# Optimization experiments

Measured on AMD Instinct MI355X. Metric: run time of the kernel, lower is better.

Reference implementation:

```python
import jax, jax.numpy as jnp
import numpy as np

B, T, D, H = 2, 2048, 1024, 16
DH = D // H

def setup_inputs() -> dict:
    key = jax.random.key(0)
    ks = jax.random.split(key, 5)
    s = 1.0 / np.sqrt(D)
    return {
        "x": jax.random.normal(ks[0], (B, T, D), dtype=jnp.float32),
        "w_q": jax.random.normal(ks[1], (D, D), dtype=jnp.float32) * s,
        "w_k": jax.random.normal(ks[2], (D, D), dtype=jnp.float32) * s,
        "w_v": jax.random.normal(ks[3], (D, D), dtype=jnp.float32) * s,
        "w_o": jax.random.normal(ks[4], (D, D), dtype=jnp.float32) * s,
    }

def reference(x, w_q, w_k, w_v, w_o):
    # Linear(bias=False): y = x @ W.T
    q = jnp.einsum('btd,ed->bte', x, w_q).reshape(B, T, H, DH).transpose(0, 2, 1, 3)
    k = jnp.einsum('btd,ed->bte', x, w_k).reshape(B, T, H, DH).transpose(0, 2, 1, 3)
    v = jnp.einsum('btd,ed->bte', x, w_v).reshape(B, T, H, DH).transpose(0, 2, 1, 3)
    scores = jnp.einsum('bhqd,bhkd->bhqk', q, k) / np.sqrt(DH)  # [B,H,T,T]
    causal = jnp.triu(jnp.ones((T, T), dtype=bool), k=1)
    scores = jnp.where(causal[None, None, :, :], -jnp.inf, scores)
    attn = jax.nn.softmax(scores, axis=-1)
    ctx = jnp.einsum('bhqk,bhkd->bhqd', attn, v)
    ctx = ctx.transpose(0, 2, 1, 3).reshape(B, T, D)
    out = jnp.einsum('btd,ed->bte', ctx, w_o)
    return out
```

## Files before the change

### kernel.cpp

```cpp
#include <hip/hip_runtime.h>
#include <hip/hip_bf16.h>

typedef __bf16 bf16_t;
typedef __attribute__((ext_vector_type(8))) __bf16 bf16x8;
typedef __attribute__((ext_vector_type(4))) __bf16 bf16x4;
typedef __attribute__((ext_vector_type(4))) float f32x4;
typedef __attribute__((ext_vector_type(16))) float f32x16;
typedef __attribute__((ext_vector_type(2))) int i32x2;

#define B_ 2
#define T_ 2048
#define D_ 1024
#define H_ 16
#define DH_ 64
#define RS_ 3072

static __device__ __forceinline__ f32x4 mfma16(bf16x8 a, bf16x8 b, f32x4 c) {
  return __builtin_amdgcn_mfma_f32_16x16x32_bf16(a, b, c, 0, 0, 0);
}
static __device__ __forceinline__ f32x16 mfma32(bf16x8 a, bf16x8 b, f32x16 c) {
  return __builtin_amdgcn_mfma_f32_32x32x16_bf16(a, b, c, 0, 0, 0);
}
static __device__ __forceinline__ void gld16(const bf16_t* g, bf16_t* l) {
  __builtin_amdgcn_global_load_lds(
      (const __attribute__((address_space(1))) unsigned int*)g,
      (__attribute__((address_space(3))) unsigned int*)l, 16, 0, 0);
}
static __device__ __forceinline__ unsigned lds_addr(const bf16_t* p) {
  return (unsigned)(uintptr_t)(const __attribute__((address_space(3))) bf16_t*)p;
}
static __device__ __forceinline__ i32x2 tr64(unsigned a) {
  i32x2 d;
  asm volatile("ds_read_b64_tr_b16 %0, %1" : "=v"(d) : "v"(a));
  return d;
}
static __device__ __forceinline__ i32x2 tr64o(unsigned a) {
  i32x2 d;
  asm volatile("ds_read_b64_tr_b16 %0, %1 offset:128" : "=v"(d) : "v"(a));
  return d;
}
static __device__ __forceinline__ unsigned pk2(float lo, float hi2) {
  unsigned short a = __builtin_bit_cast(unsigned short, (bf16_t)lo);
  unsigned short b = __builtin_bit_cast(unsigned short, (bf16_t)hi2);
  return (unsigned)a | ((unsigned)b << 16);
}

#define WAITV3 { asm volatile("s_waitcnt vmcnt(3)" ::: "memory"); __builtin_amdgcn_sched_barrier(0); }
#define WAITV4 { asm volatile("s_waitcnt vmcnt(4)" ::: "memory"); __builtin_amdgcn_sched_barrier(0); }
#define WAITV0 { asm volatile("s_waitcnt vmcnt(0)" ::: "memory"); __builtin_amdgcn_sched_barrier(0); }
#define BAR    { __builtin_amdgcn_s_barrier(); __builtin_amdgcn_sched_barrier(0); }
#define WAITL0 { asm volatile("s_waitcnt lgkmcnt(0)" ::: "memory"); __builtin_amdgcn_sched_barrier(0); }

__global__ __launch_bounds__(256) void cvt_all(const float* __restrict__ x,
                                               const float* __restrict__ w0,
                                               const float* __restrict__ w1,
                                               const float* __restrict__ w2,
                                               const float* __restrict__ w3,
                                               bf16_t* __restrict__ out) {
  const int y = blockIdx.y;
  const float* in = (y < 4) ? (x + (size_t)y * 1048576)
                            : (y == 4 ? w0 : y == 5 ? w1 : y == 6 ? w2 : w3);
  bf16_t* o = out + (size_t)y * 1048576;
  int i = blockIdx.x * 256 + threadIdx.x;
  float4 f = reinterpret_cast<const float4*>(in)[i];
  bf16x4 v;
  v[0] = (bf16_t)f.x; v[1] = (bf16_t)f.y; v[2] = (bf16_t)f.z; v[3] = (bf16_t)f.w;
  reinterpret_cast<bf16x4*>(o)[i] = v;
}

template <bool STORE_F32, bool QSCALE>
__global__ __launch_bounds__(256) void gemm_nt(const bf16_t* __restrict__ A,
                                               const bf16_t* __restrict__ Bm,
                                               void* __restrict__ Cv,
                                               int M, int N, int K, int nbx) {
  __shared__ __align__(16) bf16_t As[3][128 * 32];
  __shared__ __align__(16) bf16_t Bs[3][128 * 32];
  const int id = blockIdx.x;
  const int nwg = gridDim.x;
  const int cpx = nwg >> 3;
  const int swz = (id & 7) * cpx + (id >> 3);
  const int bx = swz % nbx, by = swz / nbx;
  const int tid = threadIdx.x, lane = tid & 63, wave = tid >> 6;
  const int l15 = lane & 15;
  const int brow = by * 128, bcol = bx * 128;
  const int row0 = (wave >> 1) * 64, col0 = (wave & 1) * 64;
  const float cscale = (QSCALE && bcol < 1024) ? 0.18033688011112042f : 1.0f;

  f32x4 acc[4][4];
#pragma unroll
  for (int m = 0; m < 4; ++m)
#pragma unroll
    for (int n = 0; n < 4; ++n) acc[m][n] = f32x4{0.f, 0.f, 0.f, 0.f};

  const int nst = K >> 5;
  const int srow = tid >> 2;
  const int sc8 = (tid & 3) * 8;
  auto stage = [&](int bi, int ks) {
    const int k0 = ks * 32;
#pragma unroll
    for (int i = 0; i < 2; ++i)
      gld16(A + (size_t)(brow + 64 * i + srow) * K + k0 + sc8,
            &As[bi][2048 * i + 512 * wave]);
#pragma unroll
    for (int i = 0; i < 2; ++i)
      gld16(Bm + (size_t)(bcol + 64 * i + srow) * K + k0 + sc8,
            &Bs[bi][2048 * i + 512 * wave]);
  };

  stage(0, 0);
  stage(1, 1);

#pragma unroll 1
  for (int ks = 0; ks < nst; ++ks) {
    if (ks + 1 < nst) { WAITV4 } else { WAITV0 }
    BAR;
    if (ks + 2 < nst) stage((ks + 2) % 3, ks + 2);

    const bf16_t* Ab = &As[ks % 3][0];
    const bf16_t* Bb = &Bs[ks % 3][0];
    const int ko = (lane >> 4) * 8;
    bf16x8 af[4], bfr[4];
#pragma unroll
    for (int m = 0; m < 4; ++m)
      af[m] = *(const bf16x8*)&Ab[(row0 + 16 * m + l15) * 32 + ko];
#pragma unroll
    for (int n = 0; n < 4; ++n)
      bfr[n] = *(const bf16x8*)&Bb[(col0 + 16 * n + l15) * 32 + ko];
    WAITL0;
#pragma unroll
    for (int m = 0; m < 4; ++m)
#pragma unroll
      for (int n = 0; n < 4; ++n) acc[m][n] = mfma16(af[m], bfr[n], acc[m][n]);
  }

  const int crow = brow + row0 + (lane >> 4) * 4;
  const int ccol = bcol + col0 + l15;
#pragma unroll
  for (int m = 0; m < 4; ++m)
#pragma unroll
    for (int n = 0; n < 4; ++n)
#pragma unroll
      for (int r = 0; r < 4; ++r) {
        size_t idx = (size_t)(crow + 16 * m + r) * N + (ccol + 16 * n);
        float v = acc[m][n][r] * cscale;
        if (STORE_F32) reinterpret_cast<float*>(Cv)[idx] = v;
        else reinterpret_cast<bf16_t*>(Cv)[idx] = (bf16_t)v;
      }
}

__global__ __launch_bounds__(256) void gemm_nt64(const bf16_t* __restrict__ A,
                                                 const bf16_t* __restrict__ Bm,
                                                 float* __restrict__ Cv,
                                                 int M, int N, int K, int nbx) {
  __shared__ __align__(16) bf16_t As[3][64 * 32];
  __shared__ __align__(16) bf16_t Bs[3][128 * 32];
  const int id = blockIdx.x;
  const int cpx = gridDim.x >> 3;
  const int swz = (id & 7) * cpx + (id >> 3);
  const int bx = swz % nbx, by = swz / nbx;
  const int tid = threadIdx.x, lane = tid & 63, wave = tid >> 6;
  const int l15 = lane & 15;
  const int brow = by * 64, bcol = bx * 128;
  const int row0 = (wave >> 1) * 32, col0 = (wave & 1) * 64;

  f32x4 acc[2][4];
#pragma unroll
  for (int m = 0; m < 2; ++m)
#pragma unroll
    for (int n = 0; n < 4; ++n) acc[m][n] = f32x4{0.f, 0.f, 0.f, 0.f};

  const int nst = K >> 5;
  const int sr = lane >> 2;
  const int sc8 = (lane & 3) * 8;
  auto stage = [&](int bi, int ks) {
    const int k0 = ks * 32;
    gld16(A + (size_t)(brow + 16 * wave + sr) * K + k0 + sc8, &As[bi][512 * wave]);
#pragma unroll
    for (int i = 0; i < 2; ++i)
      gld16(Bm + (size_t)(bcol + 64 * i + 16 * wave + sr) * K + k0 + sc8,
            &Bs[bi][2048 * i + 512 * wave]);
  };

  stage(0, 0);
  stage(1, 1);

#pragma unroll 1
  for (int ks = 0; ks < nst; ++ks) {
    if (ks + 1 < nst) { WAITV3 } else { WAITV0 }
    BAR;
    if (ks + 2 < nst) stage((ks + 2) % 3, ks + 2);

    const bf16_t* Ab = &As[ks % 3][0];
    const bf16_t* Bb = &Bs[ks % 3][0];
    const int ko = (lane >> 4) * 8;
    bf16x8 af[2], bfr[4];
#pragma unroll
    for (int m = 0; m < 2; ++m)
      af[m] = *(const bf16x8*)&Ab[(row0 + 16 * m + l15) * 32 + ko];
#pragma unroll
    for (int n = 0; n < 4; ++n)
      bfr[n] = *(const bf16x8*)&Bb[(col0 + 16 * n + l15) * 32 + ko];
    WAITL0;
#pragma unroll
    for (int m = 0; m < 2; ++m)
#pragma unroll
      for (int n = 0; n < 4; ++n) acc[m][n] = mfma16(af[m], bfr[n], acc[m][n]);
  }

  const int crow = brow + row0 + (lane >> 4) * 4;
  const int ccol = bcol + col0 + l15;
#pragma unroll
  for (int m = 0; m < 2; ++m)
#pragma unroll
    for (int n = 0; n < 4; ++n)
#pragma unroll
      for (int r = 0; r < 4; ++r)
        Cv[(size_t)(crow + 16 * m + r) * N + (ccol + 16 * n)] = acc[m][n][r];
}

#define CROW(r) ((((r) & 3) + 8 * ((r) >> 2)) + 4 * hi)

__global__ __launch_bounds__(256, 1) void attn_fwd(const bf16_t* __restrict__ qkv,
                                                   bf16_t* __restrict__ ctx) {
  __shared__ __align__(128) bf16_t KV[3][2][64 * 64];
  const int tid = threadIdx.x;
  const int lane = tid & 63;
  const int wv = tid >> 6;
  const int bh = blockIdx.x, p = blockIdx.y;
  const int b = bh >> 4, h = bh & 15;
  const bf16_t* Qg = qkv + (size_t)b * T_ * RS_ + h * DH_;
  const bf16_t* Kg = Qg + 1024;
  const bf16_t* Vg = Qg + 2048;
  bf16_t* Cg = ctx + (size_t)b * T_ * D_ + h * DH_;

  const int hi = lane >> 5;
  const int l31 = lane & 31;
  const int l15 = lane & 15;

  auto stage = [&](int bi, int kt) {
    bf16_t* Kb = &KV[bi][0][0];
    bf16_t* Vb = &KV[bi][1][0];
#pragma unroll
    for (int i = 0; i < 2; ++i) {
      int c2 = i * 256 + tid;
      int r = c2 >> 3, g8 = (c2 & 7) ^ (r & 7);
      gld16(Kg + (size_t)(kt * 64 + r) * RS_ + g8 * 8, Kb + i * 2048 + wv * 512);
    }
#pragma unroll
    for (int i = 0; i < 2; ++i) {
      int c2 = i * 256 + tid;
      int pn = c2 >> 7, k = (c2 >> 1) & 63, half = c2 & 1;
      gld16(Vg + (size_t)(kt * 64 + k) * RS_ + pn * 16 + half * 8, Vb + i * 2048 + wv * 512);
    }
  };

#pragma unroll 1
  for (int phase = 0; phase < 2; ++phase) {
    const int c = phase ? (63 - 4 * p - wv) : (4 * p + wv);
    const int q0 = c * 32;
    const int mynkt = (c >> 1) + 1;
    const int maxnkt = phase ? (32 - 2 * p) : (2 * p + 2);

    BAR;
    stage(0, 0);
    stage(1, 1);

    bf16x8 qf[4];
#pragma unroll
    for (int d = 0; d < 4; ++d)
      qf[d] = *(const bf16x8*)&Qg[(size_t)(q0 + l31) * RS_ + d * 16 + hi * 8];

    f32x16 o[2];
#pragma unroll
    for (int n = 0; n < 2; ++n)
#pragma unroll
      for (int r = 0; r < 16; ++r) o[n][r] = 0.f;
    float mrow = -1e30f, lsum = 0.f;

#pragma unroll 1
    for (int kt = 0; kt < maxnkt; ++kt) {
      if (kt + 1 < maxnkt) { WAITV4 } else { WAITV0 }
      BAR;
      if (kt + 2 < maxnkt) stage((kt + 2) % 3, kt + 2);

      if (kt < mynkt) {
        const bf16_t* Kb = &KV[kt % 3][0][0];
        bf16x8 kf[2][4];
#pragma unroll
        for (int t = 0; t < 2; ++t)
#pragma unroll
          for (int d = 0; d < 4; ++d) {
            int row = 32 * t + l31;
            int col = ((d * 2 + hi) ^ (row & 7)) * 8;
            kf[t][d] = *(const bf16x8*)&Kb[row * 64 + col];
          }
        bf16x8 vf[2][4];
        {
          unsigned vb = lds_addr(&KV[kt % 3][1][0]);
#pragma unroll
          for (int n2 = 0; n2 < 2; ++n2)
#pragma unroll
            for (int ks = 0; ks < 4; ++ks) {
              int pn = 2 * n2 + (l31 >> 4);
              int k0 = ks * 16 + hi * 8;
              unsigned a = vb + pn * 2048 + k0 * 32 + l15 * 8;
              i32x2 lo = tr64(a);
              i32x2 hi4 = tr64o(a);
              union { unsigned u[4]; bf16x8 v; } uu;
              uu.u[0] = (unsigned)lo[0]; uu.u[1] = (unsigned)lo[1];
              uu.u[2] = (unsigned)hi4[0]; uu.u[3] = (unsigned)hi4[1];
              vf[n2][ks] = uu.v;
            }
        }
        WAITL0;

        f32x16 st[2];
#pragma unroll
        for (int t = 0; t < 2; ++t) {
#pragma unroll
          for (int r = 0; r < 16; ++r) st[t][r] = 0.f;
#pragma unroll
          for (int d = 0; d < 4; ++d) st[t] = mfma32(kf[t][d], qf[d], st[t]);
        }
        if (kt == mynkt - 1) {
#pragma unroll
          for (int t = 0; t < 2; ++t)
#pragma unroll
            for (int r = 0; r < 16; ++r)
              if (kt * 64 + 32 * t + CROW(r) > q0 + l31) st[t][r] = -1e30f;
        }
        float pm = -1e30f;
#pragma unroll
        for (int t = 0; t < 2; ++t)
#pragma unroll
          for (int r = 0; r < 16; ++r) pm = fmaxf(pm, st[t][r]);
        pm = fmaxf(pm, __shfl_xor(pm, 32));
        if (!__all(pm - mrow <= 11.0f)) {
          float mn = fmaxf(mrow, pm);
          float scl = exp2f(mrow - mn);
          mrow = mn;
          lsum *= scl;
#pragma unroll
          for (int r = 0; r < 16; ++r) {
            float sr = __shfl(scl, CROW(r));
            o[0][r] *= sr;
            o[1][r] *= sr;
          }
        }
        float ps = 0.f;
#pragma unroll
        for (int t = 0; t < 2; ++t)
#pragma unroll
          for (int r = 0; r < 16; ++r) {
            float e = exp2f(st[t][r] - mrow);
            st[t][r] = e;
            ps += e;
          }
        ps += __shfl_xor(ps, 32);
        lsum += ps;
        unsigned pk[2][8];
#pragma unroll
        for (int t = 0; t < 2; ++t)
#pragma unroll
          for (int j = 0; j < 8; ++j) pk[t][j] = pk2(st[t][2 * j], st[t][2 * j + 1]);
#pragma unroll
        for (int ks = 0; ks < 4; ++ks) {
          const int t = ks >> 1, rb = (ks & 1) * 4;
          unsigned s0 = hi ? pk[t][rb] : pk[t][rb + 2];
          unsigned s1 = hi ? pk[t][rb + 1] : pk[t][rb + 3];
          unsigned r0 = (unsigned)__shfl_xor((int)s0, 32);
          unsigned r1 = (unsigned)__shfl_xor((int)s1, 32);
          union { unsigned u[4]; bf16x8 v; } w;
          if (hi == 0) {
            w.u[0] = pk[t][rb]; w.u[1] = pk[t][rb + 1]; w.u[2] = r0; w.u[3] = r1;
          } else {
            w.u[0] = r0; w.u[1] = r1; w.u[2] = pk[t][rb + 2]; w.u[3] = pk[t][rb + 3];
          }
          o[0] = mfma32(w.v, vf[0][ks], o[0]);
          o[1] = mfma32(w.v, vf[1][ks], o[1]);
        }
      }
    }

#pragma unroll
    for (int r = 0; r < 16; ++r) {
      float li = __shfl(lsum, CROW(r));
      float inv = 1.0f / li;
      int qrow = q0 + CROW(r);
#pragma unroll
      for (int n2 = 0; n2 < 2; ++n2)
        Cg[(size_t)qrow * D_ + n2 * 32 + l31] = (bf16_t)(o[n2][r] * inv);
    }
  }
}

extern "C" void kernel_launch(void* const* d_in, const int* in_sizes, int n_in,
                              void* d_out, int out_size, void* d_ws, size_t ws_size,
                              hipStream_t stream) {
  const float* x   = (const float*)d_in[0];
  const float* w_q = (const float*)d_in[1];
  const float* w_k = (const float*)d_in[2];
  const float* w_v = (const float*)d_in[3];
  const float* w_o = (const float*)d_in[4];

  const int M = B_ * T_;
  const size_t XN = (size_t)M * D_;
  const size_t WN = (size_t)D_ * D_;

  bf16_t* ws = (bf16_t*)d_ws;
  bf16_t* xb   = ws;
  bf16_t* wqb  = xb + XN;
  bf16_t* wob  = wqb + 3 * WN;
  bf16_t* qkv  = wob + WN;
  bf16_t* ctx  = qkv + (size_t)M * RS_;

  cvt_all<<<dim3(1024, 8), 256, 0, stream>>>(x, w_q, w_k, w_v, w_o, ws);

  gemm_nt<false, true><<<768, 256, 0, stream>>>(xb, wqb, qkv, M, RS_, D_, RS_ / 128);

  attn_fwd<<<dim3(B_ * H_, 8), 256, 0, stream>>>(qkv, ctx);

  gemm_nt64<<<512, 256, 0, stream>>>(ctx, wob, (float*)d_out, M, D_, D_, D_ / 128);
}
```

Measured before the change: 132.0 us.

## Process two KV tiles per pipeline step in causal attention loop

The attention kernel now stages and processes pairs of 64-key tiles per iteration, so the key block per step grows to 128. Each pair pays one barrier, one wait and one online-softmax max/rescale instead of two. This halves synchronisation and rescale overhead. In exchange it doubles LDS use to 96KB, raises register pressure from holding two score tiles, and can waste work on a partly masked second tile.

```diff
diff --git a/kernel.cpp b/kernel.cpp
--- a/kernel.cpp
+++ b/kernel.cpp
@@ -47,6 +47,7 @@
 
 #define WAITV3 { asm volatile("s_waitcnt vmcnt(3)" ::: "memory"); __builtin_amdgcn_sched_barrier(0); }
 #define WAITV4 { asm volatile("s_waitcnt vmcnt(4)" ::: "memory"); __builtin_amdgcn_sched_barrier(0); }
+#define WAITV8 { asm volatile("s_waitcnt vmcnt(8)" ::: "memory"); __builtin_amdgcn_sched_barrier(0); }
 #define WAITV0 { asm volatile("s_waitcnt vmcnt(0)" ::: "memory"); __builtin_amdgcn_sched_barrier(0); }
 #define BAR    { __builtin_amdgcn_s_barrier(); __builtin_amdgcn_sched_barrier(0); }
 #define WAITL0 { asm volatile("s_waitcnt lgkmcnt(0)" ::: "memory"); __builtin_amdgcn_sched_barrier(0); }
@@ -222,7 +223,7 @@
 
 __global__ __launch_bounds__(256, 1) void attn_fwd(const bf16_t* __restrict__ qkv,
                                                    bf16_t* __restrict__ ctx) {
-  __shared__ __align__(128) bf16_t KV[3][2][64 * 64];
+  __shared__ __align__(128) bf16_t KV[3][2][2][4096];
   const int tid = threadIdx.x;
   const int lane = tid & 63;
   const int wv = tid >> 6;
@@ -237,9 +238,9 @@
   const int l31 = lane & 31;
   const int l15 = lane & 15;
 
-  auto stage = [&](int bi, int kt) {
-    bf16_t* Kb = &KV[bi][0][0];
-    bf16_t* Vb = &KV[bi][1][0];
+  auto stage_t = [&](int bi, int tp, int kt) {
+    bf16_t* Kb = &KV[bi][tp][0][0];
+    bf16_t* Vb = &KV[bi][tp][1][0];
 #pragma unroll
     for (int i = 0; i < 2; ++i) {
       int c2 = i * 256 + tid;
@@ -259,11 +260,12 @@
     const int c = phase ? (63 - 4 * p - wv) : (4 * p + wv);
     const int q0 = c * 32;
     const int mynkt = (c >> 1) + 1;
-    const int maxnkt = phase ? (32 - 2 * p) : (2 * p + 2);
+    const int maxp = phase ? (16 - p) : (p + 1);
 
     BAR;
-    stage(0, 0);
-    stage(1, 1);
+    stage_t(0, 0, 0);
+    stage_t(0, 1, 1);
+    if (maxp > 1) { stage_t(1, 0, 2); stage_t(1, 1, 3); }
 
     bf16x8 qf[4];
 #pragma unroll
@@ -278,13 +280,20 @@
     float mrow = -1e30f, lsum = 0.f;
 
 #pragma unroll 1
-    for (int kt = 0; kt < maxnkt; ++kt) {
-      if (kt + 1 < maxnkt) { WAITV4 } else { WAITV0 }
+    for (int pi = 0; pi < maxp; ++pi) {
+      if (pi + 1 < maxp) { WAITV8 } else { WAITV0 }
       BAR;
-      if (kt + 2 < maxnkt) stage((kt + 2) % 3, kt + 2);
-
-      if (kt < mynkt) {
-        const bf16_t* Kb = &KV[kt % 3][0][0];
+      if (pi + 2 < maxp) {
+        stage_t((pi + 2) % 3, 0, 2 * (pi + 2));
+        stage_t((pi + 2) % 3, 1, 2 * (pi + 2) + 1);
+      }
+
+      const int t0 = 2 * pi, t1 = 2 * pi + 1;
+      const bool act1 = t1 < mynkt;
+
+      f32x16 st0[2], st1[2];
+      {
+        const bf16_t* Kb = &KV[pi % 3][0][0][0];
         bf16x8 kf[2][4];
 #pragma unroll
         for (int t = 0; t < 2; ++t)
@@ -294,75 +303,117 @@
             int col = ((d * 2 + hi) ^ (row & 7)) * 8;
             kf[t][d] = *(const bf16x8*)&Kb[row * 64 + col];
           }
+#pragma unroll
+        for (int t = 0; t < 2; ++t) {
+#pragma unroll
+          for (int r = 0; r < 16; ++r) st0[t][r] = 0.f;
+#pragma unroll
+          for (int d = 0; d < 4; ++d) st0[t] = mfma32(kf[t][d], qf[d], st0[t]);
+        }
+      }
+      if (t0 == mynkt - 1) {
+#pragma unroll
+        for (int t = 0; t < 2; ++t)
+#pragma unroll
+          for (int r = 0; r < 16; ++r)
+            if (t0 * 64 + 32 * t + CROW(r) > q0 + l31) st0[t][r] = -1e30f;
+      }
+      if (act1) {
+        const bf16_t* Kb = &KV[pi % 3][1][0][0];
+        bf16x8 kf[2][4];
+#pragma unroll
+        for (int t = 0; t < 2; ++t)
+#pragma unroll
+          for (int d = 0; d < 4; ++d) {
+            int row = 32 * t + l31;
+            int col = ((d * 2 + hi) ^ (row & 7)) * 8;
+            kf[t][d] = *(const bf16x8*)&Kb[row * 64 + col];
+          }
+#pragma unroll
+        for (int t = 0; t < 2; ++t) {
+#pragma unroll
+          for (int r = 0; r < 16; ++r) st1[t][r] = 0.f;
+#pragma unroll
+          for (int d = 0; d < 4; ++d) st1[t] = mfma32(kf[t][d], qf[d], st1[t]);
+        }
+        if (t1 == mynkt - 1) {
+#pragma unroll
+          for (int t = 0; t < 2; ++t)
+#pragma unroll
+            for (int r = 0; r < 16; ++r)
+              if (t1 * 64 + 32 * t + CROW(r) > q0 + l31) st1[t][r] = -1e30f;
+        }
+      }
+
+      float pm = -1e30f;
+#pragma unroll
+      for (int t = 0; t < 2; ++t)
+#pragma unroll
+        for (int r = 0; r < 16; ++r) pm = fmaxf(pm, st0[t][r]);
+      if (act1) {
+#pragma unroll
+        for (int t = 0; t < 2; ++t)
+#pragma unroll
+          for (int r = 0; r < 16; ++r) pm = fmaxf(pm, st1[t][r]);
+      }
+      pm = fmaxf(pm, __shfl_xor(pm, 32));
+      if (!__all(pm - mrow <= 11.0f)) {
+        float mn = fmaxf(mrow, pm);
+        float scl = exp2f(mrow - mn);
+        mrow = mn;
+        lsum *= scl;
+#pragma unroll
+        for (int r = 0; r < 16; ++r) {
+          float sr = __shfl(scl, CROW(r));
+          o[0][r] *= sr;
+          o[1][r] *= sr;
+        }
+      }
+      float ps = 0.f;
+#pragma unroll
+      for (int t = 0; t < 2; ++t)
+#pragma unroll
+        for (int r = 0; r < 16; ++r) {
+          float e = exp2f(st0[t][r] - mrow);
+          st0[t][r] = e;
+          ps += e;
+        }
+      if (act1) {
+#pragma unroll
+        for (int t = 0; t < 2; ++t)
+#pragma unroll
+          for (int r = 0; r < 16; ++r) {
+            float e = exp2f(st1[t][r] - mrow);
+            st1[t][r] = e;
+            ps += e;
+          }
+      }
+      ps += __shfl_xor(ps, 32);
+      lsum += ps;
+
+      {
+        unsigned pk[2][8];
+#pragma unroll
+        for (int t = 0; t < 2; ++t)
+#pragma unroll
+          for (int j = 0; j < 8; ++j) pk[t][j] = pk2(st0[t][2 * j], st0[t][2 * j + 1]);
         bf16x8 vf[2][4];
-        {
-          unsigned vb = lds_addr(&KV[kt % 3][1][0]);
-#pragma unroll
-          for (int n2 = 0; n2 < 2; ++n2)
-#pragma unroll
-            for (int ks = 0; ks < 4; ++ks) {
-              int pn = 2 * n2 + (l31 >> 4);
-              int k0 = ks * 16 + hi * 8;
-              unsigned a = vb + pn * 2048 + k0 * 32 + l15 * 8;
-              i32x2 lo = tr64(a);
-              i32x2 hi4 = tr64o(a);
-              union { unsigned u[4]; bf16x8 v; } uu;
-              uu.u[0] = (unsigned)lo[0]; uu.u[1] = (unsigned)lo[1];
-              uu.u[2] = (unsigned)hi4[0]; uu.u[3] = (unsigned)hi4[1];
-              vf[n2][ks] = uu.v;
-            }
-        }
+        unsigned vb = lds_addr(&KV[pi % 3][0][1][0]);
+#pragma unroll
+        for (int n2 = 0; n2 < 2; ++n2)
+#pragma unroll
+          for (int ks = 0; ks < 4; ++ks) {
+            int pn = 2 * n2 + (l31 >> 4);
+            int k0 = ks * 16 + hi * 8;
+            unsigned a = vb + pn * 2048 + k0 * 32 + l15 * 8;
+            i32x2 lo = tr64(a);
+            i32x2 hi4 = tr64o(a);
+            union { unsigned u[4]; bf16x8 v; } uu;
+            uu.u[0] = (unsigned)lo[0]; uu.u[1] = (unsigned)lo[1];
+            uu.u[2] = (unsigned)hi4[0]; uu.u[3] = (unsigned)hi4[1];
+            vf[n2][ks] = uu.v;
+          }
         WAITL0;
-
-        f32x16 st[2];
-#pragma unroll
-        for (int t = 0; t < 2; ++t) {
-#pragma unroll
-          for (int r = 0; r < 16; ++r) st[t][r] = 0.f;
-#pragma unroll
-          for (int d = 0; d < 4; ++d) st[t] = mfma32(kf[t][d], qf[d], st[t]);
-        }
-        if (kt == mynkt - 1) {
-#pragma unroll
-          for (int t = 0; t < 2; ++t)
-#pragma unroll
-            for (int r = 0; r < 16; ++r)
-              if (kt * 64 + 32 * t + CROW(r) > q0 + l31) st[t][r] = -1e30f;
-        }
-        float pm = -1e30f;
-#pragma unroll
-        for (int t = 0; t < 2; ++t)
-#pragma unroll
-          for (int r = 0; r < 16; ++r) pm = fmaxf(pm, st[t][r]);
-        pm = fmaxf(pm, __shfl_xor(pm, 32));
-        if (!__all(pm - mrow <= 11.0f)) {
-          float mn = fmaxf(mrow, pm);
-          float scl = exp2f(mrow - mn);
-          mrow = mn;
-          lsum *= scl;
-#pragma unroll
-          for (int r = 0; r < 16; ++r) {
-            float sr = __shfl(scl, CROW(r));
-            o[0][r] *= sr;
-            o[1][r] *= sr;
-          }
-        }
-        float ps = 0.f;
-#pragma unroll
-        for (int t = 0; t < 2; ++t)
-#pragma unroll
-          for (int r = 0; r < 16; ++r) {
-            float e = exp2f(st[t][r] - mrow);
-            st[t][r] = e;
-            ps += e;
-          }
-        ps += __shfl_xor(ps, 32);
-        lsum += ps;
-        unsigned pk[2][8];
-#pragma unroll
-        for (int t = 0; t < 2; ++t)
-#pragma unroll
-          for (int j = 0; j < 8; ++j) pk[t][j] = pk2(st[t][2 * j], st[t][2 * j + 1]);
 #pragma unroll
         for (int ks = 0; ks < 4; ++ks) {
           const int t = ks >> 1, rb = (ks & 1) * 4;
@@ -380,6 +431,46 @@
           o[1] = mfma32(w.v, vf[1][ks], o[1]);
         }
       }
+      if (act1) {
+        unsigned pk[2][8];
+#pragma unroll
+        for (int t = 0; t < 2; ++t)
+#pragma unroll
+          for (int j = 0; j < 8; ++j) pk[t][j] = pk2(st1[t][2 * j], st1[t][2 * j + 1]);
+        bf16x8 vf[2][4];
+        unsigned vb = lds_addr(&KV[pi % 3][1][1][0]);
+#pragma unroll
+        for (int n2 = 0; n2 < 2; ++n2)
+#pragma unroll
+          for (int ks = 0; ks < 4; ++ks) {
+            int pn = 2 * n2 + (l31 >> 4);
+            int k0 = ks * 16 + hi * 8;
+            unsigned a = vb + pn * 2048 + k0 * 32 + l15 * 8;
+            i32x2 lo = tr64(a);
+            i32x2 hi4 = tr64o(a);
+            union { unsigned u[4]; bf16x8 v; } uu;
+            uu.u[0] = (unsigned)lo[0]; uu.u[1] = (unsigned)lo[1];
+            uu.u[2] = (unsigned)hi4[0]; uu.u[3] = (unsigned)hi4[1];
+            vf[n2][ks] = uu.v;
+          }
+        WAITL0;
+#pragma unroll
+        for (int ks = 0; ks < 4; ++ks) {
+          const int t = ks >> 1, rb = (ks & 1) * 4;
+          unsigned s0 = hi ? pk[t][rb] : pk[t][rb + 2];
+          unsigned s1 = hi ? pk[t][rb + 1] : pk[t][rb + 3];
+          unsigned r0 = (unsigned)__shfl_xor((int)s0, 32);
+          unsigned r1 = (unsigned)__shfl_xor((int)s1, 32);
+          union { unsigned u[4]; bf16x8 v; } w;
+          if (hi == 0) {
+            w.u[0] = pk[t][rb]; w.u[1] = pk[t][rb + 1]; w.u[2] = r0; w.u[3] = r1;
+          } else {
+            w.u[0] = r0; w.u[1] = r1; w.u[2] = pk[t][rb + 2]; w.u[3] = pk[t][rb + 3];
+          }
+          o[0] = mfma32(w.v, vf[0][ks], o[0]);
+          o[1] = mfma32(w.v, vf[1][ks], o[1]);
+        }
+      }
     }
 
 #pragma unroll
```

After: 125.4 us, median of 2. 1.05x faster.

## Process four KV tiles per iteration with double-buffered 256-key stages

Applied to the files above, without the earlier changes.

Restructures the attention inner loop to stage four 64-key K/V tiles at once into a double buffer and run one online-softmax max/rescale over 256 keys instead of 64. This cuts barriers, wait points and softmax rescale passes per key, and gives more independent MFMA work to interleave. In exchange LDS use grows to 128 KB, register pressure rises sharply (four score tiles live at once, risking spills), and causal tiles are handled at coarser granularity, so some waves idle longer at the boundary.

```diff
diff --git a/kernel.cpp b/kernel.cpp
--- a/kernel.cpp
+++ b/kernel.cpp
@@ -47,6 +47,7 @@
 
 #define WAITV3 { asm volatile("s_waitcnt vmcnt(3)" ::: "memory"); __builtin_amdgcn_sched_barrier(0); }
 #define WAITV4 { asm volatile("s_waitcnt vmcnt(4)" ::: "memory"); __builtin_amdgcn_sched_barrier(0); }
+#define WAITV16 { asm volatile("s_waitcnt vmcnt(16)" ::: "memory"); __builtin_amdgcn_sched_barrier(0); }
 #define WAITV0 { asm volatile("s_waitcnt vmcnt(0)" ::: "memory"); __builtin_amdgcn_sched_barrier(0); }
 #define BAR    { __builtin_amdgcn_s_barrier(); __builtin_amdgcn_sched_barrier(0); }
 #define WAITL0 { asm volatile("s_waitcnt lgkmcnt(0)" ::: "memory"); __builtin_amdgcn_sched_barrier(0); }
@@ -222,7 +223,7 @@
 
 __global__ __launch_bounds__(256, 1) void attn_fwd(const bf16_t* __restrict__ qkv,
                                                    bf16_t* __restrict__ ctx) {
-  __shared__ __align__(128) bf16_t KV[3][2][64 * 64];
+  __shared__ __align__(128) bf16_t KV[2][4][2][4096];
   const int tid = threadIdx.x;
   const int lane = tid & 63;
   const int wv = tid >> 6;
@@ -237,9 +238,9 @@
   const int l31 = lane & 31;
   const int l15 = lane & 15;
 
-  auto stage = [&](int bi, int kt) {
-    bf16_t* Kb = &KV[bi][0][0];
-    bf16_t* Vb = &KV[bi][1][0];
+  auto stage_t = [&](int bi, int tq, int kt) {
+    bf16_t* Kb = &KV[bi][tq][0][0];
+    bf16_t* Vb = &KV[bi][tq][1][0];
 #pragma unroll
     for (int i = 0; i < 2; ++i) {
       int c2 = i * 256 + tid;
@@ -253,17 +254,20 @@
       gld16(Vg + (size_t)(kt * 64 + k) * RS_ + pn * 16 + half * 8, Vb + i * 2048 + wv * 512);
     }
   };
+  auto stage_q = [&](int bi, int qi) {
+#pragma unroll
+    for (int tq = 0; tq < 4; ++tq) stage_t(bi, tq, 4 * qi + tq);
+  };
 
 #pragma unroll 1
   for (int phase = 0; phase < 2; ++phase) {
     const int c = phase ? (63 - 4 * p - wv) : (4 * p + wv);
     const int q0 = c * 32;
     const int mynkt = (c >> 1) + 1;
-    const int maxnkt = phase ? (32 - 2 * p) : (2 * p + 2);
+    const int maxq = phase ? ((16 - p + 1) >> 1) : ((p + 2) >> 1);
 
     BAR;
-    stage(0, 0);
-    stage(1, 1);
+    stage_q(0, 0);
 
     bf16x8 qf[4];
 #pragma unroll
@@ -278,25 +282,100 @@
     float mrow = -1e30f, lsum = 0.f;
 
 #pragma unroll 1
-    for (int kt = 0; kt < maxnkt; ++kt) {
-      if (kt + 1 < maxnkt) { WAITV4 } else { WAITV0 }
+    for (int qi = 0; qi < maxq; ++qi) {
       BAR;
-      if (kt + 2 < maxnkt) stage((kt + 2) % 3, kt + 2);
-
-      if (kt < mynkt) {
-        const bf16_t* Kb = &KV[kt % 3][0][0];
-        bf16x8 kf[2][4];
-#pragma unroll
-        for (int t = 0; t < 2; ++t)
-#pragma unroll
-          for (int d = 0; d < 4; ++d) {
-            int row = 32 * t + l31;
-            int col = ((d * 2 + hi) ^ (row & 7)) * 8;
-            kf[t][d] = *(const bf16x8*)&Kb[row * 64 + col];
+      if (qi + 1 < maxq) {
+        stage_q((qi + 1) & 1, qi + 1);
+        WAITV16;
+      } else {
+        WAITV0;
+      }
+
+      const int bi = qi & 1;
+      bool act[4];
+#pragma unroll
+      for (int tq = 0; tq < 4; ++tq) act[tq] = (4 * qi + tq) < mynkt;
+
+      f32x16 st[4][2];
+#pragma unroll
+      for (int tq = 0; tq < 4; ++tq) {
+        if (act[tq]) {
+          const bf16_t* Kb = &KV[bi][tq][0][0];
+          bf16x8 kf[2][4];
+#pragma unroll
+          for (int t = 0; t < 2; ++t)
+#pragma unroll
+            for (int d = 0; d < 4; ++d) {
+              int row = 32 * t + l31;
+              int col = ((d * 2 + hi) ^ (row & 7)) * 8;
+              kf[t][d] = *(const bf16x8*)&Kb[row * 64 + col];
+            }
+#pragma unroll
+          for (int t = 0; t < 2; ++t) {
+#pragma unroll
+            for (int r = 0; r < 16; ++r) st[tq][t][r] = 0.f;
+#pragma unroll
+            for (int d = 0; d < 4; ++d) st[tq][t] = mfma32(kf[t][d], qf[d], st[tq][t]);
           }
-        bf16x8 vf[2][4];
-        {
-          unsigned vb = lds_addr(&KV[kt % 3][1][0]);
+          if (4 * qi + tq == mynkt - 1) {
+#pragma unroll
+            for (int t = 0; t < 2; ++t)
+#pragma unroll
+              for (int r = 0; r < 16; ++r)
+                if ((4 * qi + tq) * 64 + 32 * t + CROW(r) > q0 + l31) st[tq][t][r] = -1e30f;
+          }
+        }
+      }
+
+      float pm = -1e30f;
+#pragma unroll
+      for (int tq = 0; tq < 4; ++tq)
+        if (act[tq])
+#pragma unroll
+          for (int t = 0; t < 2; ++t)
+#pragma unroll
+            for (int r = 0; r < 16; ++r) pm = fmaxf(pm, st[tq][t][r]);
+      pm = fmaxf(pm, __shfl_xor(pm, 32));
+      if (!__all(pm - mrow <= 11.0f)) {
+        float mn = fmaxf(mrow, pm);
+        float scl = exp2f(mrow - mn);
+        mrow = mn;
+        lsum *= scl;
+#pragma unroll
+        for (int r = 0; r < 16; ++r) {
+          float sr = __shfl(scl, CROW(r));
+          o[0][r] *= sr;
+          o[1][r] *= sr;
+        }
+      }
+      unsigned pkq[4][2][8];
+      float ps = 0.f;
+#pragma unroll
+      for (int tq = 0; tq < 4; ++tq) {
+        if (act[tq]) {
+#pragma unroll
+          for (int t = 0; t < 2; ++t)
+#pragma unroll
+            for (int r = 0; r < 16; ++r) {
+              float e = exp2f(st[tq][t][r] - mrow);
+              st[tq][t][r] = e;
+              ps += e;
+            }
+#pragma unroll
+          for (int t = 0; t < 2; ++t)
+#pragma unroll
+            for (int j = 0; j < 8; ++j)
+              pkq[tq][t][j] = pk2(st[tq][t][2 * j], st[tq][t][2 * j + 1]);
+        }
+      }
+      ps += __shfl_xor(ps, 32);
+      lsum += ps;
+
+#pragma unroll
+      for (int tq = 0; tq < 4; ++tq) {
+        if (act[tq]) {
+          bf16x8 vf[2][4];
+          unsigned vb = lds_addr(&KV[bi][tq][1][0]);
 #pragma unroll
           for (int n2 = 0; n2 < 2; ++n2)
 #pragma unroll
@@ -311,73 +390,23 @@
               uu.u[2] = (unsigned)hi4[0]; uu.u[3] = (unsigned)hi4[1];
               vf[n2][ks] = uu.v;
             }
-        }
-        WAITL0;
-
-        f32x16 st[2];
-#pragma unroll
-        for (int t = 0; t < 2; ++t) {
-#pragma unroll
-          for (int r = 0; r < 16; ++r) st[t][r] = 0.f;
-#pragma unroll
-          for (int d = 0; d < 4; ++d) st[t] = mfma32(kf[t][d], qf[d], st[t]);
-        }
-        if (kt == mynkt - 1) {
-#pragma unroll
-          for (int t = 0; t < 2; ++t)
-#pragma unroll
-            for (int r = 0; r < 16; ++r)
-              if (kt * 64 + 32 * t + CROW(r) > q0 + l31) st[t][r] = -1e30f;
-        }
-        float pm = -1e30f;
-#pragma unroll
-        for (int t = 0; t < 2; ++t)
-#pragma unroll
-          for (int r = 0; r < 16; ++r) pm = fmaxf(pm, st[t][r]);
-        pm = fmaxf(pm, __shfl_xor(pm, 32));
-        if (!__all(pm - mrow <= 11.0f)) {
-          float mn = fmaxf(mrow, pm);
-          float scl = exp2f(mrow - mn);
-          mrow = mn;
-          lsum *= scl;
-#pragma unroll
-          for (int r = 0; r < 16; ++r) {
-            float sr = __shfl(scl, CROW(r));
-            o[0][r] *= sr;
-            o[1][r] *= sr;
+          WAITL0;
+#pragma unroll
+          for (int ks = 0; ks < 4; ++ks) {
+            const int t = ks >> 1, rb = (ks & 1) * 4;
+            unsigned s0 = hi ? pkq[tq][t][rb] : pkq[tq][t][rb + 2];
+            unsigned s1 = hi ? pkq[tq][t][rb + 1] : pkq[tq][t][rb + 3];
+            unsigned r0 = (unsigned)__shfl_xor((int)s0, 32);
+            unsigned r1 = (unsigned)__shfl_xor((int)s1, 32);
+            union { unsigned u[4]; bf16x8 v; } w;
+            if (hi == 0) {
+              w.u[0] = pkq[tq][t][rb]; w.u[1] = pkq[tq][t][rb + 1]; w.u[2] = r0; w.u[3] = r1;
+            } else {
+              w.u[0] = r0; w.u[1] = r1; w.u[2] = pkq[tq][t][rb + 2]; w.u[3] = pkq[tq][t][rb + 3];
+            }
+            o[0] = mfma32(w.v, vf[0][ks], o[0]);
+            o[1] = mfma32(w.v, vf[1][ks], o[1]);
           }
-        }
-        float ps = 0.f;
-#pragma unroll
-        for (int t = 0; t < 2; ++t)
-#pragma unroll
-          for (int r = 0; r < 16; ++r) {
-            float e = exp2f(st[t][r] - mrow);
-            st[t][r] = e;
-            ps += e;
-          }
-        ps += __shfl_xor(ps, 32);
-        lsum += ps;
-        unsigned pk[2][8];
-#pragma unroll
-        for (int t = 0; t < 2; ++t)
-#pragma unroll
-          for (int j = 0; j < 8; ++j) pk[t][j] = pk2(st[t][2 * j], st[t][2 * j + 1]);
-#pragma unroll
-        for (int ks = 0; ks < 4; ++ks) {
-          const int t = ks >> 1, rb = (ks & 1) * 4;
-          unsigned s0 = hi ? pk[t][rb] : pk[t][rb + 2];
-          unsigned s1 = hi ? pk[t][rb + 1] : pk[t][rb + 3];
-          unsigned r0 = (unsigned)__shfl_xor((int)s0, 32);
-          unsigned r1 = (unsigned)__shfl_xor((int)s1, 32);
-          union { unsigned u[4]; bf16x8 v; } w;
-          if (hi == 0) {
-            w.u[0] = pk[t][rb]; w.u[1] = pk[t][rb + 1]; w.u[2] = r0; w.u[3] = r1;
-          } else {
-            w.u[0] = r0; w.u[1] = r1; w.u[2] = pk[t][rb + 2]; w.u[3] = pk[t][rb + 3];
-          }
-          o[0] = mfma32(w.v, vf[0][ks], o[0]);
-          o[1] = mfma32(w.v, vf[1][ks], o[1]);
         }
       }
     }
```

Result: no change. 132.4 us (+0.4%).

## Process three KV tiles per barrier step with double-buffered triple staging

Applied to the files above, without the earlier changes.

Restructures the attention inner loop so each iteration stages and processes three 64-key tiles at once, double-buffering groups of three tiles in LDS. The online-softmax max and rescale now happen once per three tiles instead of once per tile. Barriers and waitcnt points drop to one per group. In exchange the block uses twice the LDS and holds more score registers live. Masking can waste work on the partial last group.

```diff
diff --git a/kernel.cpp b/kernel.cpp
--- a/kernel.cpp
+++ b/kernel.cpp
@@ -47,6 +47,7 @@
 
 #define WAITV3 { asm volatile("s_waitcnt vmcnt(3)" ::: "memory"); __builtin_amdgcn_sched_barrier(0); }
 #define WAITV4 { asm volatile("s_waitcnt vmcnt(4)" ::: "memory"); __builtin_amdgcn_sched_barrier(0); }
+#define WAITV12 { asm volatile("s_waitcnt vmcnt(12)" ::: "memory"); __builtin_amdgcn_sched_barrier(0); }
 #define WAITV0 { asm volatile("s_waitcnt vmcnt(0)" ::: "memory"); __builtin_amdgcn_sched_barrier(0); }
 #define BAR    { __builtin_amdgcn_s_barrier(); __builtin_amdgcn_sched_barrier(0); }
 #define WAITL0 { asm volatile("s_waitcnt lgkmcnt(0)" ::: "memory"); __builtin_amdgcn_sched_barrier(0); }
@@ -222,7 +223,7 @@
 
 __global__ __launch_bounds__(256, 1) void attn_fwd(const bf16_t* __restrict__ qkv,
                                                    bf16_t* __restrict__ ctx) {
-  __shared__ __align__(128) bf16_t KV[3][2][64 * 64];
+  __shared__ __align__(128) bf16_t KV[2][3][2][4096];
   const int tid = threadIdx.x;
   const int lane = tid & 63;
   const int wv = tid >> 6;
@@ -237,9 +238,9 @@
   const int l31 = lane & 31;
   const int l15 = lane & 15;
 
-  auto stage = [&](int bi, int kt) {
-    bf16_t* Kb = &KV[bi][0][0];
-    bf16_t* Vb = &KV[bi][1][0];
+  auto stage_t = [&](int bi, int tp, int kt) {
+    bf16_t* Kb = &KV[bi][tp][0][0];
+    bf16_t* Vb = &KV[bi][tp][1][0];
 #pragma unroll
     for (int i = 0; i < 2; ++i) {
       int c2 = i * 256 + tid;
@@ -253,17 +254,20 @@
       gld16(Vg + (size_t)(kt * 64 + k) * RS_ + pn * 16 + half * 8, Vb + i * 2048 + wv * 512);
     }
   };
+  auto stage_3 = [&](int bi, int ti) {
+#pragma unroll
+    for (int j = 0; j < 3; ++j) stage_t(bi, j, 3 * ti + j);
+  };
 
 #pragma unroll 1
   for (int phase = 0; phase < 2; ++phase) {
     const int c = phase ? (63 - 4 * p - wv) : (4 * p + wv);
     const int q0 = c * 32;
     const int mynkt = (c >> 1) + 1;
-    const int maxnkt = phase ? (32 - 2 * p) : (2 * p + 2);
+    const int maxp3 = phase ? ((34 - 2 * p) / 3) : ((2 * p + 4) / 3);
 
     BAR;
-    stage(0, 0);
-    stage(1, 1);
+    stage_3(0, 0);
 
     bf16x8 qf[4];
 #pragma unroll
@@ -278,62 +282,61 @@
     float mrow = -1e30f, lsum = 0.f;
 
 #pragma unroll 1
-    for (int kt = 0; kt < maxnkt; ++kt) {
-      if (kt + 1 < maxnkt) { WAITV4 } else { WAITV0 }
+    for (int pi = 0; pi < maxp3; ++pi) {
       BAR;
-      if (kt + 2 < maxnkt) stage((kt + 2) % 3, kt + 2);
-
-      if (kt < mynkt) {
-        const bf16_t* Kb = &KV[kt % 3][0][0];
-        bf16x8 kf[2][4];
-#pragma unroll
-        for (int t = 0; t < 2; ++t)
-#pragma unroll
-          for (int d = 0; d < 4; ++d) {
-            int row = 32 * t + l31;
-            int col = ((d * 2 + hi) ^ (row & 7)) * 8;
-            kf[t][d] = *(const bf16x8*)&Kb[row * 64 + col];
+      if (pi + 1 < maxp3) {
+        stage_3((pi + 1) & 1, pi + 1);
+        WAITV12;
+      } else {
+        WAITV0;
+      }
+
+      const int bi = pi & 1;
+      const int tb = 3 * pi;
+      if (tb < mynkt) {
+        bool act[3];
+#pragma unroll
+        for (int j = 0; j < 3; ++j) act[j] = (tb + j) < mynkt;
+
+        f32x16 st[3][2];
+#pragma unroll
+        for (int j = 0; j < 3; ++j) {
+          if (act[j]) {
+            const bf16_t* Kb = &KV[bi][j][0][0];
+            bf16x8 kf[2][4];
+#pragma unroll
+            for (int t = 0; t < 2; ++t)
+#pragma unroll
+              for (int d = 0; d < 4; ++d) {
+                int row = 32 * t + l31;
+                int col = ((d * 2 + hi) ^ (row & 7)) * 8;
+                kf[t][d] = *(const bf16x8*)&Kb[row * 64 + col];
+              }
+#pragma unroll
+            for (int t = 0; t < 2; ++t) {
+#pragma unroll
+              for (int r = 0; r < 16; ++r) st[j][t][r] = 0.f;
+#pragma unroll
+              for (int d = 0; d < 4; ++d) st[j][t] = mfma32(kf[t][d], qf[d], st[j][t]);
+            }
+            if (tb + j == mynkt - 1) {
+#pragma unroll
+              for (int t = 0; t < 2; ++t)
+#pragma unroll
+                for (int r = 0; r < 16; ++r)
+                  if ((tb + j) * 64 + 32 * t + CROW(r) > q0 + l31) st[j][t][r] = -1e30f;
+            }
           }
-        bf16x8 vf[2][4];
-        {
-          unsigned vb = lds_addr(&KV[kt % 3][1][0]);
-#pragma unroll
-          for (int n2 = 0; n2 < 2; ++n2)
-#pragma unroll
-            for (int ks = 0; ks < 4; ++ks) {
-              int pn = 2 * n2 + (l31 >> 4);
-              int k0 = ks * 16 + hi * 8;
-              unsigned a = vb + pn * 2048 + k0 * 32 + l15 * 8;
-              i32x2 lo = tr64(a);
-              i32x2 hi4 = tr64o(a);
-              union { unsigned u[4]; bf16x8 v; } uu;
-              uu.u[0] = (unsigned)lo[0]; uu.u[1] = (unsigned)lo[1];
-              uu.u[2] = (unsigned)hi4[0]; uu.u[3] = (unsigned)hi4[1];
-              vf[n2][ks] = uu.v;
-            }
         }
-        WAITL0;
-
-        f32x16 st[2];
-#pragma unroll
-        for (int t = 0; t < 2; ++t) {
-#pragma unroll
-          for (int r = 0; r < 16; ++r) st[t][r] = 0.f;
-#pragma unroll
-          for (int d = 0; d < 4; ++d) st[t] = mfma32(kf[t][d], qf[d], st[t]);
-        }
-        if (kt == mynkt - 1) {
-#pragma unroll
-          for (int t = 0; t < 2; ++t)
-#pragma unroll
-            for (int r = 0; r < 16; ++r)
-              if (kt * 64 + 32 * t + CROW(r) > q0 + l31) st[t][r] = -1e30f;
-        }
+
         float pm = -1e30f;
 #pragma unroll
-        for (int t = 0; t < 2; ++t)
-#pragma unroll
-          for (int r = 0; r < 16; ++r) pm = fmaxf(pm, st[t][r]);
+        for (int j = 0; j < 3; ++j)
+          if (act[j])
+#pragma unroll
+            for (int t = 0; t < 2; ++t)
+#pragma unroll
+              for (int r = 0; r < 16; ++r) pm = fmaxf(pm, st[j][t][r]);
         pm = fmaxf(pm, __shfl_xor(pm, 32));
         if (!__all(pm - mrow <= 11.0f)) {
           float mn = fmaxf(mrow, pm);
@@ -347,38 +350,62 @@
             o[1][r] *= sr;
           }
         }
+
         float ps = 0.f;
 #pragma unroll
-        for (int t = 0; t < 2; ++t)
-#pragma unroll
-          for (int r = 0; r < 16; ++r) {
-            float e = exp2f(st[t][r] - mrow);
-            st[t][r] = e;
-            ps += e;
+        for (int j = 0; j < 3; ++j) {
+          if (act[j]) {
+#pragma unroll
+            for (int t = 0; t < 2; ++t)
+#pragma unroll
+              for (int r = 0; r < 16; ++r) {
+                float e = exp2f(st[j][t][r] - mrow);
+                st[j][t][r] = e;
+                ps += e;
+              }
+            unsigned pk[2][8];
+#pragma unroll
+            for (int t = 0; t < 2; ++t)
+#pragma unroll
+              for (int jj = 0; jj < 8; ++jj)
+                pk[t][jj] = pk2(st[j][t][2 * jj], st[j][t][2 * jj + 1]);
+            bf16x8 vf[2][4];
+            unsigned vb = lds_addr(&KV[bi][j][1][0]);
+#pragma unroll
+            for (int n2 = 0; n2 < 2; ++n2)
+#pragma unroll
+              for (int ks = 0; ks < 4; ++ks) {
+                int pn = 2 * n2 + (l31 >> 4);
+                int k0 = ks * 16 + hi * 8;
+                unsigned a = vb + pn * 2048 + k0 * 32 + l15 * 8;
+                i32x2 lo = tr64(a);
+                i32x2 hi4 = tr64o(a);
+                union { unsigned u[4]; bf16x8 v; } uu;
+                uu.u[0] = (unsigned)lo[0]; uu.u[1] = (unsigned)lo[1];
+                uu.u[2] = (unsigned)hi4[0]; uu.u[3] = (unsigned)hi4[1];
+                vf[n2][ks] = uu.v;
+              }
+            WAITL0;
+#pragma unroll
+            for (int ks = 0; ks < 4; ++ks) {
+              const int t = ks >> 1, rb = (ks & 1) * 4;
+              unsigned s0 = hi ? pk[t][rb] : pk[t][rb + 2];
+              unsigned s1 = hi ? pk[t][rb + 1] : pk[t][rb + 3];
+              unsigned r0 = (unsigned)__shfl_xor((int)s0, 32);
+              unsigned r1 = (unsigned)__shfl_xor((int)s1, 32);
+              union { unsigned u[4]; bf16x8 v; } w;
+              if (hi == 0) {
+                w.u[0] = pk[t][rb]; w.u[1] = pk[t][rb + 1]; w.u[2] = r0; w.u[3] = r1;
+              } else {
+                w.u[0] = r0; w.u[1] = r1; w.u[2] = pk[t][rb + 2]; w.u[3] = pk[t][rb + 3];
+              }
+              o[0] = mfma32(w.v, vf[0][ks], o[0]);
+              o[1] = mfma32(w.v, vf[1][ks], o[1]);
+            }
           }
+        }
         ps += __shfl_xor(ps, 32);
         lsum += ps;
-        unsigned pk[2][8];
-#pragma unroll
-        for (int t = 0; t < 2; ++t)
-#pragma unroll
-          for (int j = 0; j < 8; ++j) pk[t][j] = pk2(st[t][2 * j], st[t][2 * j + 1]);
-#pragma unroll
-        for (int ks = 0; ks < 4; ++ks) {
-          const int t = ks >> 1, rb = (ks & 1) * 4;
-          unsigned s0 = hi ? pk[t][rb] : pk[t][rb + 2];
-          unsigned s1 = hi ? pk[t][rb + 1] : pk[t][rb + 3];
-          unsigned r0 = (unsigned)__shfl_xor((int)s0, 32);
-          unsigned r1 = (unsigned)__shfl_xor((int)s1, 32);
-          union { unsigned u[4]; bf16x8 v; } w;
-          if (hi == 0) {
-            w.u[0] = pk[t][rb]; w.u[1] = pk[t][rb + 1]; w.u[2] = r0; w.u[3] = r1;
-          } else {
-            w.u[0] = r0; w.u[1] = r1; w.u[2] = pk[t][rb + 2]; w.u[3] = pk[t][rb + 3];
-          }
-          o[0] = mfma32(w.v, vf[0][ks], o[0]);
-          o[1] = mfma32(w.v, vf[1][ks], o[1]);
-        }
       }
     }
 
```

New measurement: 129.6 us. Within noise of the previous version (-1.8%).
